# Optimization experiments

Hardware: AMD Instinct MI355X
Metric: run time of the kernel (lower is better)

Reference implementation:

```python
import jax, jax.numpy as jnp
import numpy as np

B, F, D = 32, 4096, 256
ALPHA = 0.001


def setup_inputs() -> dict:
    key = jax.random.key(0)
    ks = jax.random.split(key, 9)
    s = 1.0 / np.sqrt(D)
    return {
        "q": jax.random.normal(ks[0], (B, F, D), dtype=jnp.float32),
        "k": jax.random.normal(ks[1], (B, F, D), dtype=jnp.float32),
        "v": jax.random.normal(ks[2], (B, F, D), dtype=jnp.float32),
        "Wq": jax.random.normal(ks[3], (D, D), dtype=jnp.float32) * s,
        "bq": jax.random.normal(ks[4], (D,), dtype=jnp.float32) * 0.01,
        "Wk": jax.random.normal(ks[5], (D, D), dtype=jnp.float32) * s,
        "bk": jax.random.normal(ks[6], (D,), dtype=jnp.float32) * 0.01,
        "Wv": jax.random.normal(ks[7], (D, D), dtype=jnp.float32) * s,
        "bv": jax.random.normal(ks[8], (D,), dtype=jnp.float32) * 0.01,
    }


def reference(q, k, v, Wq, bq, Wk, bk, Wv, bv):
    # nn.Linear: x @ W.T + b
    queries = q @ Wq.T + bq            # [b, f, d]
    keys = k @ Wk.T + bk               # [b, f, d]
    values = v @ Wv.T + bv             # [b, f, d]
    # batched Gram matrix + ridge term
    key_sym = jnp.einsum("bfd,bfe->bde", keys, keys)          # [b, d, d]
    key_sym = key_sym + ALPHA * jnp.eye(D, dtype=key_sym.dtype)
    key_sym_inv = jnp.linalg.inv(key_sym)                      # [b, d, d]
    kkik = jnp.einsum("bde,bfe->bdf", key_sym_inv, keys)       # [b, d, f]
    kkikv = jnp.einsum("bdf,bfe->bde", kkik, values)           # [b, d, d]
    itn = jax.nn.softmax(kkikv, axis=2)                        # sigma=True; softmax over dim 2
    h = jnp.einsum("bfd,bde->be", queries, itn)                # [b, d]
    return h
```

## Files before the change

### kernel.cpp

```cpp
#include <hip/hip_runtime.h>
#include <math.h>

#define FDIM 4096
#define DDIM 256
#define ALPHA_R 0.001f

typedef __attribute__((ext_vector_type(8))) short short8;
typedef __attribute__((ext_vector_type(4))) float f32x4;

__device__ __forceinline__ unsigned cvt_pk_bf16(float lo_e, float hi_e) {
  unsigned r;
  asm("v_cvt_pk_bf16_f32 %0, %1, %2" : "=v"(r) : "v"(lo_e), "v"(hi_e));
  return r;
}

__global__ void colsum_partial_q(const float* __restrict__ q,
                                 float* __restrict__ part) {
  int chunk = blockIdx.x;
  int b     = blockIdx.y;
  int tid = threadIdx.x;
  int rg = tid >> 6, dq = tid & 63;
  const float* p = q + ((size_t)b * FDIM + chunk * 256 + rg) * DDIM + dq * 4;
  float4 s = make_float4(0.f, 0.f, 0.f, 0.f);
  for (int i = 0; i < 64; ++i) {
    float4 t = *(const float4*)(p + (size_t)i * 4 * DDIM);
    s.x += t.x; s.y += t.y; s.z += t.z; s.w += t.w;
  }
  __shared__ __align__(16) float red[4][64][4];
  *(float4*)&red[rg][dq][0] = s;
  __syncthreads();
  if (rg == 0) {
    float4 a0 = *(float4*)&red[0][dq][0];
    float4 a1 = *(float4*)&red[1][dq][0];
    float4 a2 = *(float4*)&red[2][dq][0];
    float4 a3 = *(float4*)&red[3][dq][0];
    float4 t = make_float4(a0.x + a1.x + a2.x + a3.x, a0.y + a1.y + a2.y + a3.y,
                           a0.z + a1.z + a2.z + a3.z, a0.w + a1.w + a2.w + a3.w);
    *(float4*)(part + ((size_t)chunk * 32 + b) * DDIM + dq * 4) = t;
  }
}

__global__ void colsum_reduce_q(const float* __restrict__ part,
                                float* __restrict__ svec) {
  int b = blockIdx.x; int d = threadIdx.x;
  float s = 0.f;
  for (int c = 0; c < 16; ++c) s += part[((size_t)c * 32 + b) * DDIM + d];
  svec[(size_t)b * DDIM + d] = s;
}

__global__ __launch_bounds__(256) void gram_mfma(const float* __restrict__ kg,
                                                 const float* __restrict__ vg,
                                                 float* __restrict__ G,
                                                 float* __restrict__ svec) {
  int flat = blockIdx.x;
  int xcd = flat & 7, s = flat >> 3;
  int b = xcd * 4 + (s >> 4);
  int tile = s & 15;
  int tm = tile >> 2, tn = tile & 3;
  int mBase = tm * 64, nBase = tn * 64;
  const float* Kb = kg + (size_t)b * FDIM * DDIM;
  const float* Vb = vg + (size_t)b * FDIM * DDIM;

  __shared__ __align__(16) unsigned short Ah[64][40], Al[64][40];
  __shared__ __align__(16) unsigned short Bh[64][40], Bl[64][40];
  __shared__ __align__(16) unsigned short Ch[64][40], Cl[64][40];
  __shared__ float sred[4][68];

  int tid = threadIdx.x;
  int w = tid >> 6, lane = tid & 63;
  int wr = w >> 1, wc = w & 1;
  int lrow = lane & 15;
  int kof = (lane >> 4) * 8;

  const float* pA = Kb + mBase + lane;
  const float* pB = Kb + nBase + lane;
  const float* pC = Vb + nBase + lane;

  bool doK = (tn == 0), doV = (tm == 0);
  float sK = 0.f, sV = 0.f;

  float xa[8], xb[8], xc[8];
  auto loadIter = [&](int it) {
    int f = it * 32 + w * 8;
#pragma unroll
    for (int j = 0; j < 8; ++j) {
      xa[j] = pA[(size_t)(f + j) * DDIM];
      xb[j] = pB[(size_t)(f + j) * DDIM];
      xc[j] = pC[(size_t)(f + j) * DDIM];
    }
  };
  auto stash = [&](const float* x, unsigned short (*H)[40], unsigned short (*L)[40]) {
    unsigned h0 = cvt_pk_bf16(x[0], x[1]);
    unsigned h1 = cvt_pk_bf16(x[2], x[3]);
    unsigned h2 = cvt_pk_bf16(x[4], x[5]);
    unsigned h3 = cvt_pk_bf16(x[6], x[7]);
    unsigned l0 = cvt_pk_bf16(x[0] - __uint_as_float(h0 << 16),
                              x[1] - __uint_as_float(h0 & 0xFFFF0000u));
    unsigned l1 = cvt_pk_bf16(x[2] - __uint_as_float(h1 << 16),
                              x[3] - __uint_as_float(h1 & 0xFFFF0000u));
    unsigned l2 = cvt_pk_bf16(x[4] - __uint_as_float(h2 << 16),
                              x[5] - __uint_as_float(h2 & 0xFFFF0000u));
    unsigned l3 = cvt_pk_bf16(x[6] - __uint_as_float(h3 << 16),
                              x[7] - __uint_as_float(h3 & 0xFFFF0000u));
    *(uint4*)&H[lane][w * 8] = make_uint4(h0, h1, h2, h3);
    *(uint4*)&L[lane][w * 8] = make_uint4(l0, l1, l2, l3);
  };

  f32x4 acc0[2][2], acc1[2][2];
#pragma unroll
  for (int mt = 0; mt < 2; ++mt)
#pragma unroll
    for (int nt = 0; nt < 2; ++nt) {
      acc0[mt][nt] = (f32x4){0.f, 0.f, 0.f, 0.f};
      acc1[mt][nt] = (f32x4){0.f, 0.f, 0.f, 0.f};
    }

  loadIter(0);
  for (int it = 0; it < 128; ++it) {
    __syncthreads();
    stash(xa, Ah, Al);
    stash(xb, Bh, Bl);
    stash(xc, Ch, Cl);
    if (doK) sK += ((xa[0] + xa[1]) + (xa[2] + xa[3])) + ((xa[4] + xa[5]) + (xa[6] + xa[7]));
    if (doV) sV += ((xc[0] + xc[1]) + (xc[2] + xc[3])) + ((xc[4] + xc[5]) + (xc[6] + xc[7]));
    __syncthreads();
    if (it < 127) loadIter(it + 1);

    short8 bh[2], bl[2], ch[2], cl[2];
#pragma unroll
    for (int nt = 0; nt < 2; ++nt) {
      int rB = wc * 32 + nt * 16 + lrow;
      bh[nt] = *(const short8*)&Bh[rB][kof];
      bl[nt] = *(const short8*)&Bl[rB][kof];
      ch[nt] = *(const short8*)&Ch[rB][kof];
      cl[nt] = *(const short8*)&Cl[rB][kof];
    }
    __builtin_amdgcn_s_setprio(1);
#pragma unroll
    for (int mt = 0; mt < 2; ++mt) {
      int rA = wr * 32 + mt * 16 + lrow;
      short8 ah = *(const short8*)&Ah[rA][kof];
      short8 al = *(const short8*)&Al[rA][kof];
#pragma unroll
      for (int nt = 0; nt < 2; ++nt) {
        f32x4 t = acc0[mt][nt];
        t = __builtin_amdgcn_mfma_f32_16x16x32_bf16(ah, bh[nt], t, 0, 0, 0);
        t = __builtin_amdgcn_mfma_f32_16x16x32_bf16(ah, bl[nt], t, 0, 0, 0);
        t = __builtin_amdgcn_mfma_f32_16x16x32_bf16(al, bh[nt], t, 0, 0, 0);
        acc0[mt][nt] = t;
        f32x4 u = acc1[mt][nt];
        u = __builtin_amdgcn_mfma_f32_16x16x32_bf16(ah, ch[nt], u, 0, 0, 0);
        u = __builtin_amdgcn_mfma_f32_16x16x32_bf16(ah, cl[nt], u, 0, 0, 0);
        u = __builtin_amdgcn_mfma_f32_16x16x32_bf16(al, ch[nt], u, 0, 0, 0);
        acc1[mt][nt] = u;
      }
    }
    __builtin_amdgcn_s_setprio(0);
  }

  float* G0 = G + ((size_t)b * 2) * 65536;
  float* G1 = G0 + 65536;
#pragma unroll
  for (int mt = 0; mt < 2; ++mt)
#pragma unroll
    for (int nt = 0; nt < 2; ++nt)
#pragma unroll
      for (int r = 0; r < 4; ++r) {
        int row = mBase + wr * 32 + mt * 16 + (lane >> 4) * 4 + r;
        int col = nBase + wc * 32 + nt * 16 + (lane & 15);
        G0[(size_t)row * DDIM + col] = acc0[mt][nt][r];
        G1[(size_t)row * DDIM + col] = acc1[mt][nt][r];
      }

  if (doK) {
    __syncthreads();
    sred[w][lane] = sK;
    __syncthreads();
    if (tid < 64) {
      float t = sred[0][tid] + sred[1][tid] + sred[2][tid] + sred[3][tid];
      svec[(size_t)1 * 32 * 256 + (size_t)b * 256 + mBase + tid] = t;
    }
  }
  if (doV) {
    __syncthreads();
    sred[w][lane] = sV;
    __syncthreads();
    if (tid < 64) {
      float t = sred[0][tid] + sred[1][tid] + sred[2][tid] + sred[3][tid];
      svec[(size_t)2 * 32 * 256 + (size_t)b * 256 + nBase + tid] = t;
    }
  }
}

__global__ void smallvec(const float* __restrict__ Wq, const float* __restrict__ bq,
                         const float* __restrict__ Wk, const float* __restrict__ Wv,
                         const float* __restrict__ svec, float* __restrict__ uvec) {
  int b = blockIdx.x; int d = threadIdx.x;
  __shared__ float sq[256], sk[256], sv[256];
  sq[d] = svec[((size_t)0 * 32 + b) * DDIM + d];
  sk[d] = svec[((size_t)1 * 32 + b) * DDIM + d];
  sv[d] = svec[((size_t)2 * 32 + b) * DDIM + d];
  __syncthreads();
  float uk = 0.f, uv = 0.f, uq = 0.f;
  for (int j = 0; j < 256; j += 4) {
    float4 wk4 = *(const float4*)(Wk + (size_t)d * DDIM + j);
    float4 wv4 = *(const float4*)(Wv + (size_t)d * DDIM + j);
    float4 wq4 = *(const float4*)(Wq + (size_t)d * DDIM + j);
    uk += wk4.x * sk[j] + wk4.y * sk[j + 1] + wk4.z * sk[j + 2] + wk4.w * sk[j + 3];
    uv += wv4.x * sv[j] + wv4.y * sv[j + 1] + wv4.z * sv[j + 2] + wv4.w * sv[j + 3];
    uq += wq4.x * sq[j] + wq4.y * sq[j + 1] + wq4.z * sq[j + 2] + wq4.w * sq[j + 3];
  }
  uvec[((size_t)0 * 32 + b) * DDIM + d] = uk;
  uvec[((size_t)1 * 32 + b) * DDIM + d] = uv;
  uvec[((size_t)2 * 32 + b) * DDIM + d] = uq + 4096.f * bq[d];
}

__global__ __launch_bounds__(256) void gemm_pass1(const float* __restrict__ Wk,
                                                  const float* __restrict__ G,
                                                  float* __restrict__ T) {
  int tile = blockIdx.x, w = blockIdx.y, b = blockIdx.z;
  int tm = tile >> 2, tn = tile & 3;
  const float* A = Wk;
  const float* B = G + ((size_t)b * 2 + w) * 65536;
  float* C = T + ((size_t)b * 2 + w) * 65536;
  __shared__ __align__(16) float As[16][64];
  __shared__ __align__(16) float Bs[16][64];
  int tid = threadIdx.x;
  int ty = tid >> 4, tx = tid & 15;
  int am = tid & 63, ak4 = tid >> 6;
  int brow = tid >> 4, bcol4 = tid & 15;
  int mBase = tm * 64, nBase = tn * 64;
  float acc[4][4];
#pragma unroll
  for (int i = 0; i < 4; i++)
#pragma unroll
    for (int j = 0; j < 4; j++) acc[i][j] = 0.f;
  for (int k0 = 0; k0 < 256; k0 += 16) {
    float4 a = *(const float4*)(A + (size_t)(mBase + am) * DDIM + k0 + ak4 * 4);
    float4 bb = *(const float4*)(B + (size_t)(k0 + brow) * DDIM + nBase + bcol4 * 4);
    __syncthreads();
    As[ak4 * 4 + 0][am] = a.x; As[ak4 * 4 + 1][am] = a.y;
    As[ak4 * 4 + 2][am] = a.z; As[ak4 * 4 + 3][am] = a.w;
    *(float4*)&Bs[brow][bcol4 * 4] = bb;
    __syncthreads();
#pragma unroll
    for (int kstep = 0; kstep < 16; ++kstep) {
      float4 a4 = *(const float4*)&As[kstep][ty * 4];
      float4 b4 = *(const float4*)&Bs[kstep][tx * 4];
      float av[4] = {a4.x, a4.y, a4.z, a4.w};
      float bvv[4] = {b4.x, b4.y, b4.z, b4.w};
#pragma unroll
      for (int i = 0; i < 4; i++)
#pragma unroll
        for (int j = 0; j < 4; j++)
          acc[i][j] = fmaf(av[i], bvv[j], acc[i][j]);
    }
  }
#pragma unroll
  for (int i = 0; i < 4; i++) {
    float4 o = make_float4(acc[i][0], acc[i][1], acc[i][2], acc[i][3]);
    *(float4*)(C + (size_t)(mBase + ty * 4 + i) * DDIM + nBase + tx * 4) = o;
  }
}

__global__ __launch_bounds__(256) void gemm_pass2(const float* __restrict__ T,
                                                  const float* __restrict__ Wk,
                                                  const float* __restrict__ Wv,
                                                  float* __restrict__ S) {
  int tile = blockIdx.x, w = blockIdx.y, b = blockIdx.z;
  int tm = tile >> 2, tn = tile & 3;
  const float* A = T + ((size_t)b * 2 + w) * 65536;
  const float* W = w ? Wv : Wk;
  float* C = S + ((size_t)b * 2 + w) * 65536;
  __shared__ __align__(16) float As[16][64];
  __shared__ __align__(16) float Bs[16][64];
  int tid = threadIdx.x;
  int ty = tid >> 4, tx = tid & 15;
  int am = tid & 63, ak4 = tid >> 6;
  int mBase = tm * 64, nBase = tn * 64;
  float acc[4][4];
#pragma unroll
  for (int i = 0; i < 4; i++)
#pragma unroll
    for (int j = 0; j < 4; j++) acc[i][j] = 0.f;
  for (int k0 = 0; k0 < 256; k0 += 16) {
    float4 a = *(const float4*)(A + (size_t)(mBase + am) * DDIM + k0 + ak4 * 4);
    float4 bb = *(const float4*)(W + (size_t)(nBase + am) * DDIM + k0 + ak4 * 4);
    __syncthreads();
    As[ak4 * 4 + 0][am] = a.x; As[ak4 * 4 + 1][am] = a.y;
    As[ak4 * 4 + 2][am] = a.z; As[ak4 * 4 + 3][am] = a.w;
    Bs[ak4 * 4 + 0][am] = bb.x; Bs[ak4 * 4 + 1][am] = bb.y;
    Bs[ak4 * 4 + 2][am] = bb.z; Bs[ak4 * 4 + 3][am] = bb.w;
    __syncthreads();
#pragma unroll
    for (int kstep = 0; kstep < 16; ++kstep) {
      float4 a4 = *(const float4*)&As[kstep][ty * 4];
      float4 b4 = *(const float4*)&Bs[kstep][tx * 4];
      float av[4] = {a4.x, a4.y, a4.z, a4.w};
      float bvv[4] = {b4.x, b4.y, b4.z, b4.w};
#pragma unroll
      for (int i = 0; i < 4; i++)
#pragma unroll
        for (int j = 0; j < 4; j++)
          acc[i][j] = fmaf(av[i], bvv[j], acc[i][j]);
    }
  }
#pragma unroll
  for (int i = 0; i < 4; i++) {
    float4 o = make_float4(acc[i][0], acc[i][1], acc[i][2], acc[i][3]);
    *(float4*)(C + (size_t)(mBase + ty * 4 + i) * DDIM + nBase + tx * 4) = o;
  }
}

__global__ void rank1(float* __restrict__ S, const float* __restrict__ uvec,
                      const float* __restrict__ bk, const float* __restrict__ bv) {
  int d = blockIdx.x, w = blockIdx.y, b = blockIdx.z;
  int e = threadIdx.x;
  float* row = S + (((size_t)b * 2 + w) * DDIM + d) * DDIM;
  float ukd = uvec[((size_t)0 * 32 + b) * DDIM + d];
  float bkd = bk[d];
  if (w == 0) {
    float uke = uvec[((size_t)0 * 32 + b) * DDIM + e];
    float add = ukd * bk[e] + bkd * uke + 4096.f * bkd * bk[e] + ((d == e) ? ALPHA_R : 0.f);
    row[e] += add;
  } else {
    float uve = uvec[((size_t)1 * 32 + b) * DDIM + e];
    float add = ukd * bv[e] + bkd * uve + 4096.f * bkd * bv[e];
    row[e] += add;
  }
}

__global__ __launch_bounds__(1024, 4) void gj_factor(float* __restrict__ Sb,
                                                     float* __restrict__ Mtg) {
  int b = blockIdx.x;
  float* A = Sb + (size_t)b * 2 * 65536;
  int tid = threadIdx.x;
  int r = tid >> 2;
  int q = tid & 3;

  __shared__ __align__(16) float Mt[64][264];
  __shared__ __align__(16) float Sst[64][200];
  __shared__ __align__(16) float prow[2][64];
  __shared__ float fac[2][256];

  for (int pg = 0; pg < 4; ++pg) {
    float x[16];
    {
      const float* Ar = A + (size_t)r * 256 + pg * 64 + q * 16;
#pragma unroll
      for (int m = 0; m < 4; ++m) {
        float4 t = *(const float4*)(Ar + m * 4);
        x[m * 4 + 0] = t.x; x[m * 4 + 1] = t.y;
        x[m * 4 + 2] = t.z; x[m * 4 + 3] = t.w;
      }
    }
    if (r == pg * 64) {
      *(float4*)&prow[0][q * 16 + 0]  = make_float4(x[0], x[1], x[2], x[3]);
      *(float4*)&prow[0][q * 16 + 4]  = make_float4(x[4], x[5], x[6], x[7]);
      *(float4*)&prow[0][q * 16 + 8]  = make_float4(x[8], x[9], x[10], x[11]);
      *(float4*)&prow[0][q * 16 + 12] = make_float4(x[12], x[13], x[14], x[15]);
    }
    if (q == 0) fac[0][r] = x[0];
    __syncthreads();

#pragma unroll
    for (int jo = 0; jo < 4; ++jo) {
#pragma unroll
      for (int ji = 0; ji < 16; ++ji) {
        const int j = jo * 16 + ji;
        const int p = pg * 64 + j;
        const int buf = j & 1, nb = buf ^ 1;
        float piv = fac[buf][p];
        float ip = 1.0f / piv;
        float g = fac[buf][r] * ip;
        bool diag = (r == p);
#pragma unroll
        for (int m = 0; m < 16; ++m) {
          float pv = prow[buf][q * 16 + m];
          x[m] = diag ? pv * ip : fmaf(-g, pv, x[m]);
        }
        if (q == jo) x[ji] = diag ? ip : (0.f - g);
        if (j < 63) {
          const int jn = j + 1;
          if (r == pg * 64 + jn) {
            *(float4*)&prow[nb][q * 16 + 0]  = make_float4(x[0], x[1], x[2], x[3]);
            *(float4*)&prow[nb][q * 16 + 4]  = make_float4(x[4], x[5], x[6], x[7]);
            *(float4*)&prow[nb][q * 16 + 8]  = make_float4(x[8], x[9], x[10], x[11]);
            *(float4*)&prow[nb][q * 16 + 12] = make_float4(x[12], x[13], x[14], x[15]);
          }
          if (q == (jn >> 4)) fac[nb][r] = x[jn & 15];
        }
        __syncthreads();
      }
    }
#pragma unroll
    for (int m = 0; m < 16; ++m) Mt[q * 16 + m][r] = x[m];
    __syncthreads();

    {
      int j = tid >> 4, rseg = (tid & 15) * 16;
      float* dst = Mtg + (((size_t)b * 4 + pg) * 64 + j) * 256 + rseg;
#pragma unroll
      for (int m = 0; m < 4; ++m) {
        float4 t = make_float4(Mt[j][rseg + m * 4 + 0], Mt[j][rseg + m * 4 + 1],
                               Mt[j][rseg + m * 4 + 2], Mt[j][rseg + m * 4 + 3]);
        *(float4*)(dst + m * 4) = t;
      }
    }

    int W = (3 - pg) * 64;
    if (W > 0) {
      int c_off = (pg + 1) * 64;
      {
        int cpt = W >> 4;
        int jr = tid >> 4, tc = tid & 15;
        const float* src = A + (size_t)(pg * 64 + jr) * 256 + c_off + tc * cpt;
        for (int m = 0; m < cpt; m += 4) {
          float4 t = *(const float4*)(src + m);
          *(float4*)&Sst[jr][tc * cpt + m] = t;
        }
      }
      __syncthreads();
      int colTiles = W >> 3;
      int rt = tid / colTiles;
      int ctile = tid - rt * colTiles;
      if (rt < 32) {
        int r0 = rt * 8, c0 = ctile * 8;
        float acc[8][8];
#pragma unroll
        for (int i = 0; i < 8; ++i)
#pragma unroll
          for (int j2 = 0; j2 < 8; ++j2) acc[i][j2] = 0.f;
        for (int j = 0; j < 64; ++j) {
          float4 m0 = *(const float4*)&Mt[j][r0];
          float4 m1 = *(const float4*)&Mt[j][r0 + 4];
          float4 s0 = *(const float4*)&Sst[j][c0];
          float4 s1 = *(const float4*)&Sst[j][c0 + 4];
          float mv[8] = {m0.x, m0.y, m0.z, m0.w, m1.x, m1.y, m1.z, m1.w};
          float sv[8] = {s0.x, s0.y, s0.z, s0.w, s1.x, s1.y, s1.z, s1.w};
#pragma unroll
          for (int i = 0; i < 8; ++i)
#pragma unroll
            for (int j2 = 0; j2 < 8; ++j2)
              acc[i][j2] = fmaf(mv[i], sv[j2], acc[i][j2]);
        }
#pragma unroll
        for (int ii = 0; ii < 8; ++ii) {
          int row = r0 + ii;
          bool inPanel = ((row >> 6) == pg);
          float* dst = A + (size_t)row * 256 + c_off + c0;
          float4 o0 = make_float4(acc[ii][0], acc[ii][1], acc[ii][2], acc[ii][3]);
          float4 o1 = make_float4(acc[ii][4], acc[ii][5], acc[ii][6], acc[ii][7]);
          if (!inPanel) {
            float4 a0 = *(const float4*)(dst);
            float4 a1 = *(const float4*)(dst + 4);
            o0.x += a0.x; o0.y += a0.y; o0.z += a0.z; o0.w += a0.w;
            o1.x += a1.x; o1.y += a1.y; o1.z += a1.z; o1.w += a1.w;
          }
          *(float4*)(dst) = o0;
          *(float4*)(dst + 4) = o1;
        }
      }
      __syncthreads();
    }
  }
}

__global__ __launch_bounds__(256) void gj_apply(float* __restrict__ Sb,
                                                const float* __restrict__ Mtg) {
  int blk = blockIdx.x;
  int b = blk >> 3;
  int cbase = (blk & 7) * 32;
  float* Bm = Sb + ((size_t)b * 2 + 1) * 65536;
  int tid = threadIdx.x;
  int rt = tid >> 3;
  int ct = tid & 7;

  __shared__ __align__(16) float Mt[64][260];
  __shared__ __align__(8) float Bp[64][34];

  float4 breg[8];
#pragma unroll
  for (int i = 0; i < 8; ++i)
    breg[i] = *(const float4*)(Bm + (size_t)(rt * 8 + i) * 256 + cbase + ct * 4);

  for (int pg = 0; pg < 4; ++pg) {
    __syncthreads();
    {
      int j = tid >> 2, seg = (tid & 3) * 64;
      const float* src = Mtg + (((size_t)b * 4 + pg) * 64 + j) * 256 + seg;
#pragma unroll
      for (int m = 0; m < 16; ++m) {
        float4 t = *(const float4*)(src + m * 4);
        *(float4*)&Mt[j][seg + m * 4] = t;
      }
    }
    if (rt >= pg * 8 && rt < (pg + 1) * 8) {
#pragma unroll
      for (int i = 0; i < 8; ++i) {
        int j = (rt - pg * 8) * 8 + i;
        *(float2*)&Bp[j][ct * 4]     = make_float2(breg[i].x, breg[i].y);
        *(float2*)&Bp[j][ct * 4 + 2] = make_float2(breg[i].z, breg[i].w);
      }
    }
    __syncthreads();

    float acc[8][4];
#pragma unroll
    for (int i = 0; i < 8; ++i)
#pragma unroll
      for (int c = 0; c < 4; ++c) acc[i][c] = 0.f;
#pragma unroll 4
    for (int j = 0; j < 64; ++j) {
      float4 m0 = *(const float4*)&Mt[j][rt * 8];
      float4 m1 = *(const float4*)&Mt[j][rt * 8 + 4];
      float2 b0 = *(const float2*)&Bp[j][ct * 4];
      float2 b1 = *(const float2*)&Bp[j][ct * 4 + 2];
      float mv[8] = {m0.x, m0.y, m0.z, m0.w, m1.x, m1.y, m1.z, m1.w};
      float bv4[4] = {b0.x, b0.y, b1.x, b1.y};
#pragma unroll
      for (int i = 0; i < 8; ++i)
#pragma unroll
        for (int c = 0; c < 4; ++c)
          acc[i][c] = fmaf(mv[i], bv4[c], acc[i][c]);
    }
    bool inPanel = ((rt >> 3) == pg);
#pragma unroll
    for (int i = 0; i < 8; ++i) {
      if (inPanel) {
        breg[i] = make_float4(acc[i][0], acc[i][1], acc[i][2], acc[i][3]);
      } else {
        breg[i].x += acc[i][0]; breg[i].y += acc[i][1];
        breg[i].z += acc[i][2]; breg[i].w += acc[i][3];
      }
    }
  }

#pragma unroll
  for (int i = 0; i < 8; ++i)
    *(float4*)(Bm + (size_t)(rt * 8 + i) * 256 + cbase + ct * 4) = breg[i];
}

__global__ void rowstats(const float* __restrict__ S, float* __restrict__ stats) {
  int b = blockIdx.x;
  const float* X = S + ((size_t)b * 2 + 1) * 65536;
  int tid = threadIdx.x; int lane = tid & 63; int wv = tid >> 6;
  for (int rr = 0; rr < 64; ++rr) {
    int row = rr * 4 + wv;
    float x0 = X[row * 256 + lane];
    float x1 = X[row * 256 + lane + 64];
    float x2 = X[row * 256 + lane + 128];
    float x3 = X[row * 256 + lane + 192];
    float m = fmaxf(fmaxf(x0, x1), fmaxf(x2, x3));
    for (int o = 32; o > 0; o >>= 1) m = fmaxf(m, __shfl_xor(m, o, 64));
    float s = expf(x0 - m) + expf(x1 - m) + expf(x2 - m) + expf(x3 - m);
    for (int o = 32; o > 0; o >>= 1) s += __shfl_xor(s, o, 64);
    if (lane == 0) {
      stats[((size_t)b * 256 + row) * 2 + 0] = m;
      stats[((size_t)b * 256 + row) * 2 + 1] = s;
    }
  }
}

__global__ void final_h(const float* __restrict__ S, const float* __restrict__ stats,
                        const float* __restrict__ uvec, float* __restrict__ out) {
  int b = blockIdx.x; int e = threadIdx.x;
  const float* X = S + ((size_t)b * 2 + 1) * 65536;
  const float* qs = uvec + ((size_t)2 * 32 + b) * DDIM;
  float acc = 0.f;
  for (int d = 0; d < 256; ++d) {
    float m = stats[((size_t)b * 256 + d) * 2 + 0];
    float s = stats[((size_t)b * 256 + d) * 2 + 1];
    acc += qs[d] * expf(X[d * 256 + e] - m) / s;
  }
  out[(size_t)b * 256 + e] = acc;
}

extern "C" void kernel_launch(void* const* d_in, const int* in_sizes, int n_in,
                              void* d_out, int out_size, void* d_ws, size_t ws_size,
                              hipStream_t stream) {
  const float* q  = (const float*)d_in[0];
  const float* k  = (const float*)d_in[1];
  const float* v  = (const float*)d_in[2];
  const float* Wq = (const float*)d_in[3];
  const float* bq = (const float*)d_in[4];
  const float* Wk = (const float*)d_in[5];
  const float* bk = (const float*)d_in[6];
  const float* Wv = (const float*)d_in[7];
  const float* bv = (const float*)d_in[8];
  float* out = (float*)d_out;

  float* ws   = (float*)d_ws;
  float* Gbuf = ws;
  float* Tbuf = Gbuf + (size_t)32 * 2 * 65536;
  float* Sbuf = Tbuf + (size_t)32 * 2 * 65536;
  float* part = Sbuf + (size_t)32 * 2 * 65536;
  float* svec = part + (size_t)16 * 3 * 32 * 256;
  float* uvec = svec + (size_t)3 * 32 * 256;
  float* stats = uvec + (size_t)3 * 32 * 256;

  colsum_partial_q<<<dim3(16, 32), 256, 0, stream>>>(q, part);
  colsum_reduce_q<<<32, 256, 0, stream>>>(part, svec);
  gram_mfma<<<512, 256, 0, stream>>>(k, v, Gbuf, svec);
  smallvec<<<32, 256, 0, stream>>>(Wq, bq, Wk, Wv, svec, uvec);
  gemm_pass1<<<dim3(16, 2, 32), 256, 0, stream>>>(Wk, Gbuf, Tbuf);
  gemm_pass2<<<dim3(16, 2, 32), 256, 0, stream>>>(Tbuf, Wk, Wv, Sbuf);
  rank1<<<dim3(256, 2, 32), 256, 0, stream>>>(Sbuf, uvec, bk, bv);
  gj_factor<<<32, 1024, 0, stream>>>(Sbuf, Gbuf);
  gj_apply<<<256, 256, 0, stream>>>(Sbuf, Gbuf);
  rowstats<<<32, 256, 0, stream>>>(Sbuf, stats);
  final_h<<<32, 256, 0, stream>>>(Sbuf, stats, uvec, out);
}
```

Baseline: 574.6 us.

## Fuse q column-sum into gram kernel, rank-1 into GEMM epilogue, softmax stages

Folds the q column-sum blocks into the gram kernel grid as extra blocks, moves the partial reduction into smallvec, and applies the rank-1 bias and ridge correction in the gemm_pass2 epilogue. The row-stats and final_h kernels are merged into one softmax_h kernel that keeps the max and scaled q in shared memory. Together this drops four kernel launches and one full read-modify-write pass over S. The cost is a larger gram grid mixing two block types, with possible load imbalance.

```diff
diff --git a/kernel.cpp b/kernel.cpp
--- a/kernel.cpp
+++ b/kernel.cpp
@@ -14,45 +14,40 @@
   return r;
 }
 
-__global__ void colsum_partial_q(const float* __restrict__ q,
-                                 float* __restrict__ part) {
-  int chunk = blockIdx.x;
-  int b     = blockIdx.y;
+__global__ __launch_bounds__(256) void gram_fused(const float* __restrict__ kg,
+                                                  const float* __restrict__ vg,
+                                                  const float* __restrict__ qg,
+                                                  float* __restrict__ G,
+                                                  float* __restrict__ svec,
+                                                  float* __restrict__ part) {
+  int flat = blockIdx.x;
   int tid = threadIdx.x;
-  int rg = tid >> 6, dq = tid & 63;
-  const float* p = q + ((size_t)b * FDIM + chunk * 256 + rg) * DDIM + dq * 4;
-  float4 s = make_float4(0.f, 0.f, 0.f, 0.f);
-  for (int i = 0; i < 64; ++i) {
-    float4 t = *(const float4*)(p + (size_t)i * 4 * DDIM);
-    s.x += t.x; s.y += t.y; s.z += t.z; s.w += t.w;
-  }
-  __shared__ __align__(16) float red[4][64][4];
-  *(float4*)&red[rg][dq][0] = s;
-  __syncthreads();
-  if (rg == 0) {
-    float4 a0 = *(float4*)&red[0][dq][0];
-    float4 a1 = *(float4*)&red[1][dq][0];
-    float4 a2 = *(float4*)&red[2][dq][0];
-    float4 a3 = *(float4*)&red[3][dq][0];
-    float4 t = make_float4(a0.x + a1.x + a2.x + a3.x, a0.y + a1.y + a2.y + a3.y,
-                           a0.z + a1.z + a2.z + a3.z, a0.w + a1.w + a2.w + a3.w);
-    *(float4*)(part + ((size_t)chunk * 32 + b) * DDIM + dq * 4) = t;
-  }
-}
-
-__global__ void colsum_reduce_q(const float* __restrict__ part,
-                                float* __restrict__ svec) {
-  int b = blockIdx.x; int d = threadIdx.x;
-  float s = 0.f;
-  for (int c = 0; c < 16; ++c) s += part[((size_t)c * 32 + b) * DDIM + d];
-  svec[(size_t)b * DDIM + d] = s;
-}
-
-__global__ __launch_bounds__(256) void gram_mfma(const float* __restrict__ kg,
-                                                 const float* __restrict__ vg,
-                                                 float* __restrict__ G,
-                                                 float* __restrict__ svec) {
-  int flat = blockIdx.x;
+
+  if (flat >= 512) {
+    int cs = flat - 512;
+    int chunk = cs & 15, b = cs >> 4;
+    int rg = tid >> 6, dq = tid & 63;
+    const float* p = qg + ((size_t)b * FDIM + chunk * 256 + rg) * DDIM + dq * 4;
+    float4 s = make_float4(0.f, 0.f, 0.f, 0.f);
+    for (int i = 0; i < 64; ++i) {
+      float4 t = *(const float4*)(p + (size_t)i * 4 * DDIM);
+      s.x += t.x; s.y += t.y; s.z += t.z; s.w += t.w;
+    }
+    __shared__ __align__(16) float redq[4][64][4];
+    *(float4*)&redq[rg][dq][0] = s;
+    __syncthreads();
+    if (rg == 0) {
+      float4 a0 = *(float4*)&redq[0][dq][0];
+      float4 a1 = *(float4*)&redq[1][dq][0];
+      float4 a2 = *(float4*)&redq[2][dq][0];
+      float4 a3 = *(float4*)&redq[3][dq][0];
+      float4 t = make_float4(a0.x + a1.x + a2.x + a3.x, a0.y + a1.y + a2.y + a3.y,
+                             a0.z + a1.z + a2.z + a3.z, a0.w + a1.w + a2.w + a3.w);
+      *(float4*)(part + ((size_t)chunk * 32 + b) * DDIM + dq * 4) = t;
+    }
+    return;
+  }
+
   int xcd = flat & 7, s = flat >> 3;
   int b = xcd * 4 + (s >> 4);
   int tile = s & 15;
@@ -66,7 +61,6 @@
   __shared__ __align__(16) unsigned short Ch[64][40], Cl[64][40];
   __shared__ float sred[4][68];
 
-  int tid = threadIdx.x;
   int w = tid >> 6, lane = tid & 63;
   int wr = w >> 1, wc = w & 1;
   int lrow = lane & 15;
@@ -194,10 +188,13 @@
 
 __global__ void smallvec(const float* __restrict__ Wq, const float* __restrict__ bq,
                          const float* __restrict__ Wk, const float* __restrict__ Wv,
+                         const float* __restrict__ part,
                          const float* __restrict__ svec, float* __restrict__ uvec) {
   int b = blockIdx.x; int d = threadIdx.x;
   __shared__ float sq[256], sk[256], sv[256];
-  sq[d] = svec[((size_t)0 * 32 + b) * DDIM + d];
+  float sqv = 0.f;
+  for (int c = 0; c < 16; ++c) sqv += part[((size_t)c * 32 + b) * DDIM + d];
+  sq[d] = sqv;
   sk[d] = svec[((size_t)1 * 32 + b) * DDIM + d];
   sv[d] = svec[((size_t)2 * 32 + b) * DDIM + d];
   __syncthreads();
@@ -266,7 +263,10 @@
 __global__ __launch_bounds__(256) void gemm_pass2(const float* __restrict__ T,
                                                   const float* __restrict__ Wk,
                                                   const float* __restrict__ Wv,
-                                                  float* __restrict__ S) {
+                                                  float* __restrict__ S,
+                                                  const float* __restrict__ uvec,
+                                                  const float* __restrict__ bk,
+                                                  const float* __restrict__ bv) {
   int tile = blockIdx.x, w = blockIdx.y, b = blockIdx.z;
   int tm = tile >> 2, tn = tile & 3;
   const float* A = T + ((size_t)b * 2 + w) * 65536;
@@ -305,28 +305,32 @@
           acc[i][j] = fmaf(av[i], bvv[j], acc[i][j]);
     }
   }
+  const float* uk = uvec + ((size_t)0 * 32 + b) * DDIM;
+  const float* uvv = uvec + ((size_t)1 * 32 + b) * DDIM;
+  float ukr[4], bkr[4], ue[4], be[4];
+#pragma unroll
+  for (int i = 0; i < 4; ++i) {
+    int row = mBase + ty * 4 + i;
+    ukr[i] = uk[row]; bkr[i] = bk[row];
+  }
+#pragma unroll
+  for (int j = 0; j < 4; ++j) {
+    int col = nBase + tx * 4 + j;
+    ue[j] = w ? uvv[col] : uk[col];
+    be[j] = w ? bv[col] : bk[col];
+  }
 #pragma unroll
   for (int i = 0; i < 4; i++) {
+    int row = mBase + ty * 4 + i;
+#pragma unroll
+    for (int j = 0; j < 4; j++) {
+      int col = nBase + tx * 4 + j;
+      float add = ukr[i] * be[j] + bkr[i] * ue[j] + 4096.f * bkr[i] * be[j];
+      if (w == 0 && row == col) add += ALPHA_R;
+      acc[i][j] += add;
+    }
     float4 o = make_float4(acc[i][0], acc[i][1], acc[i][2], acc[i][3]);
-    *(float4*)(C + (size_t)(mBase + ty * 4 + i) * DDIM + nBase + tx * 4) = o;
-  }
-}
-
-__global__ void rank1(float* __restrict__ S, const float* __restrict__ uvec,
-                      const float* __restrict__ bk, const float* __restrict__ bv) {
-  int d = blockIdx.x, w = blockIdx.y, b = blockIdx.z;
-  int e = threadIdx.x;
-  float* row = S + (((size_t)b * 2 + w) * DDIM + d) * DDIM;
-  float ukd = uvec[((size_t)0 * 32 + b) * DDIM + d];
-  float bkd = bk[d];
-  if (w == 0) {
-    float uke = uvec[((size_t)0 * 32 + b) * DDIM + e];
-    float add = ukd * bk[e] + bkd * uke + 4096.f * bkd * bk[e] + ((d == e) ? ALPHA_R : 0.f);
-    row[e] += add;
-  } else {
-    float uve = uvec[((size_t)1 * 32 + b) * DDIM + e];
-    float add = ukd * bv[e] + bkd * uve + 4096.f * bkd * bv[e];
-    row[e] += add;
+    *(float4*)(C + (size_t)row * DDIM + nBase + tx * 4) = o;
   }
 }
 
@@ -541,10 +545,15 @@
     *(float4*)(Bm + (size_t)(rt * 8 + i) * 256 + cbase + ct * 4) = breg[i];
 }
 
-__global__ void rowstats(const float* __restrict__ S, float* __restrict__ stats) {
+__global__ void softmax_h(const float* __restrict__ S,
+                          const float* __restrict__ uvec,
+                          float* __restrict__ out) {
   int b = blockIdx.x;
   const float* X = S + ((size_t)b * 2 + 1) * 65536;
   int tid = threadIdx.x; int lane = tid & 63; int wv = tid >> 6;
+  __shared__ float mrow[256], qos[256];
+  __shared__ float qs_s[256];
+  qs_s[tid] = uvec[((size_t)2 * 32 + b) * DDIM + tid];
   for (int rr = 0; rr < 64; ++rr) {
     int row = rr * 4 + wv;
     float x0 = X[row * 256 + lane];
@@ -556,23 +565,17 @@
     float s = expf(x0 - m) + expf(x1 - m) + expf(x2 - m) + expf(x3 - m);
     for (int o = 32; o > 0; o >>= 1) s += __shfl_xor(s, o, 64);
     if (lane == 0) {
-      stats[((size_t)b * 256 + row) * 2 + 0] = m;
-      stats[((size_t)b * 256 + row) * 2 + 1] = s;
-    }
-  }
-}
-
-__global__ void final_h(const float* __restrict__ S, const float* __restrict__ stats,
-                        const float* __restrict__ uvec, float* __restrict__ out) {
-  int b = blockIdx.x; int e = threadIdx.x;
-  const float* X = S + ((size_t)b * 2 + 1) * 65536;
-  const float* qs = uvec + ((size_t)2 * 32 + b) * DDIM;
+      mrow[row] = m;
+      qos[row] = s;
+    }
+  }
+  __syncthreads();
+  qos[tid] = qs_s[tid] / qos[tid];
+  __syncthreads();
+  int e = tid;
   float acc = 0.f;
-  for (int d = 0; d < 256; ++d) {
-    float m = stats[((size_t)b * 256 + d) * 2 + 0];
-    float s = stats[((size_t)b * 256 + d) * 2 + 1];
-    acc += qs[d] * expf(X[d * 256 + e] - m) / s;
-  }
+  for (int d = 0; d < 256; ++d)
+    acc += qos[d] * expf(X[d * 256 + e] - mrow[d]);
   out[(size_t)b * 256 + e] = acc;
 }
 
@@ -597,17 +600,12 @@
   float* part = Sbuf + (size_t)32 * 2 * 65536;
   float* svec = part + (size_t)16 * 3 * 32 * 256;
   float* uvec = svec + (size_t)3 * 32 * 256;
-  float* stats = uvec + (size_t)3 * 32 * 256;
-
-  colsum_partial_q<<<dim3(16, 32), 256, 0, stream>>>(q, part);
-  colsum_reduce_q<<<32, 256, 0, stream>>>(part, svec);
-  gram_mfma<<<512, 256, 0, stream>>>(k, v, Gbuf, svec);
-  smallvec<<<32, 256, 0, stream>>>(Wq, bq, Wk, Wv, svec, uvec);
+
+  gram_fused<<<1024, 256, 0, stream>>>(k, v, q, Gbuf, svec, part);
+  smallvec<<<32, 256, 0, stream>>>(Wq, bq, Wk, Wv, part, svec, uvec);
   gemm_pass1<<<dim3(16, 2, 32), 256, 0, stream>>>(Wk, Gbuf, Tbuf);
-  gemm_pass2<<<dim3(16, 2, 32), 256, 0, stream>>>(Tbuf, Wk, Wv, Sbuf);
-  rank1<<<dim3(256, 2, 32), 256, 0, stream>>>(Sbuf, uvec, bk, bv);
+  gemm_pass2<<<dim3(16, 2, 32), 256, 0, stream>>>(Tbuf, Wk, Wv, Sbuf, uvec, bk, bv);
   gj_factor<<<32, 1024, 0, stream>>>(Sbuf, Gbuf);
   gj_apply<<<256, 256, 0, stream>>>(Sbuf, Gbuf);
-  rowstats<<<32, 256, 0, stream>>>(Sbuf, stats);
-  final_h<<<32, 256, 0, stream>>>(Sbuf, stats, uvec, out);
-}
+  softmax_h<<<32, 256, 0, stream>>>(Sbuf, uvec, out);
+}
```

Result: faster. 533.4 us (-7.2%).
